# Kernel optimization log

Hardware: AMD Instinct MI355X
Metric: run time of the kernel (lower is better)

Reference implementation:

```python
import jax, jax.numpy as jnp
import numpy as np

N = 100000
E = 1600000
IN_DIM = 128
HEADS = 8
OUT_PER_HEAD = 16  # output_dim // heads = 128 // 8
NEG_SLOPE = 0.2    # PyG GATConv default negative_slope


def setup_inputs() -> dict:
    key = jax.random.key(0)
    k_x, k_ei, k_w, k_as, k_ad, k_b = jax.random.split(key, 6)
    x = jax.random.normal(k_x, (N, IN_DIM), dtype=jnp.float32)
    edge_index = jax.random.randint(k_ei, (2, E), 0, N, dtype=jnp.int64)
    # GATConv params (Glorot-ish scale)
    scale = 1.0 / np.sqrt(IN_DIM)
    W = jax.random.normal(k_w, (IN_DIM, HEADS, OUT_PER_HEAD), dtype=jnp.float32) * scale
    a_src = jax.random.normal(k_as, (HEADS, OUT_PER_HEAD), dtype=jnp.float32) * scale
    a_dst = jax.random.normal(k_ad, (HEADS, OUT_PER_HEAD), dtype=jnp.float32) * scale
    bias = jnp.zeros((HEADS * OUT_PER_HEAD,), dtype=jnp.float32)
    return {"x": x, "edge_index": edge_index, "W": W, "a_src": a_src,
            "a_dst": a_dst, "bias": bias}


def reference(x, edge_index, W, a_src, a_dst, bias):
    # Linear projection per head: [N, H, F]
    xp = jnp.einsum('ni,ihf->nhf', x, W)
    # Per-node attention halves: [N, H]
    al_src = jnp.einsum('nhf,hf->nh', xp, a_src)
    al_dst = jnp.einsum('nhf,hf->nh', xp, a_dst)
    src, dst = edge_index[0], edge_index[1]
    # Edge logits with LeakyReLU: [E, H]
    e = al_src[src] + al_dst[dst]
    e = jnp.where(e >= 0, e, NEG_SLOPE * e)
    # Segment softmax over incoming edges of each dst node
    m = jnp.full((N, HEADS), -jnp.inf, dtype=e.dtype).at[dst].max(e)
    ex = jnp.exp(e - m[dst])
    denom = jnp.zeros((N, HEADS), dtype=e.dtype).at[dst].add(ex)
    alpha = ex / jnp.where(denom[dst] == 0, 1.0, denom[dst])  # [E, H]
    # Weighted scatter-aggregate of source messages: [N, H, F]
    out = jnp.zeros((N, HEADS, OUT_PER_HEAD), dtype=xp.dtype)
    out = out.at[dst].add(xp[src] * alpha[:, :, None])
    # Concat heads, bias, ELU (GATLayer applies F.elu)
    out = out.reshape(N, HEADS * OUT_PER_HEAD) + bias
    return jnp.where(out > 0, out, jnp.expm1(out))
```

## Files before the change

kernel.cpp:

```cpp
#include <hip/hip_runtime.h>
#include <hip/hip_fp16.h>
#include <cstdint>

constexpr int IN_DIM = 128;
constexpr int OUT_DIM = 128;
constexpr int HEADS = 8;
constexpr float NEG_SLOPE = 0.2f;

constexpr int BUCKET_CAP = 2560;
constexpr int BIN_TILE   = 2048;

typedef _Float16 f16x8 __attribute__((ext_vector_type(8)));
typedef float    f32x4 __attribute__((ext_vector_type(4)));

__global__ void wa_kernel(const float* __restrict__ W, const float* __restrict__ a_src,
                          const float* __restrict__ a_dst, __half* __restrict__ wa) {
  int k = threadIdx.x;
  if (k < 128) {
#pragma unroll
    for (int h = 0; h < 8; ++h) {
      float s = 0.f, d = 0.f;
#pragma unroll
      for (int f = 0; f < 16; ++f) {
        float w = W[k * 128 + h * 16 + f];
        s += w * a_src[h * 16 + f];
        d += w * a_dst[h * 16 + f];
      }
      wa[k * 16 + h]     = __float2half(s);
      wa[k * 16 + 8 + h] = __float2half(d);
    }
  }
}

__global__ __launch_bounds__(256) void proj_kernel(
    const float* __restrict__ x, const float* __restrict__ W,
    const __half* __restrict__ wa, __half* __restrict__ xp,
    float* __restrict__ als, float* __restrict__ ald, int N)
{
  __shared__ __half xs[64 * 128];
  __shared__ __half Wt[144 * 128];
  const int t  = threadIdx.x;
  const int r0 = blockIdx.x * 64;

#pragma unroll
  for (int it = 0; it < 4; ++it) {
    int m   = t + it * 256;
    int row = m >> 4;
    int g   = m & 15;
    int grow = r0 + row;
    float4 v0 = make_float4(0.f,0.f,0.f,0.f), v1 = v0;
    if (grow < N) {
      const float* src = &x[(size_t)grow * IN_DIM + g * 8];
      v0 = *(const float4*)src;
      v1 = *(const float4*)(src + 4);
    }
    union { __half2 h2[4]; uint4 u; } u;
    u.h2[0] = __floats2half2_rn(v0.x, v0.y);
    u.h2[1] = __floats2half2_rn(v0.z, v0.w);
    u.h2[2] = __floats2half2_rn(v1.x, v1.y);
    u.h2[3] = __floats2half2_rn(v1.z, v1.w);
    *(uint4*)&xs[row * 128 + ((g ^ (row & 15)) << 3)] = u.u;
  }
#pragma unroll
  for (int it = 0; it < 16; ++it) {
    int m  = t + it * 256;
    int c  = m & 127;
    int kq = m >> 7;
    int k  = kq * 4;
    float w0 = W[(size_t)(k + 0) * OUT_DIM + c];
    float w1 = W[(size_t)(k + 1) * OUT_DIM + c];
    float w2 = W[(size_t)(k + 2) * OUT_DIM + c];
    float w3 = W[(size_t)(k + 3) * OUT_DIM + c];
    union { __half2 h2[2]; uint2 u; } u;
    u.h2[0] = __floats2half2_rn(w0, w1);
    u.h2[1] = __floats2half2_rn(w2, w3);
    int g = k >> 3;
    *(uint2*)&Wt[c * 128 + (((g ^ (c & 15)) << 3) + (k & 7))] = u.u;
  }
#pragma unroll
  for (int it = 0; it < 2; ++it) {
    int m  = t + it * 256;
    int c  = m & 15;
    int kq = m >> 4;
    int k  = kq * 4;
    union { __half h[4]; uint2 u; } u;
    u.h[0] = wa[(k + 0) * 16 + c];
    u.h[1] = wa[(k + 1) * 16 + c];
    u.h[2] = wa[(k + 2) * 16 + c];
    u.h[3] = wa[(k + 3) * 16 + c];
    int cc = 128 + c;
    int g = k >> 3;
    *(uint2*)&Wt[cc * 128 + (((g ^ (cc & 15)) << 3) + (k & 7))] = u.u;
  }
  __syncthreads();

  const int wv = t >> 6;
  const int l  = t & 63;
  const int fr = l & 15;
  const int fq = l >> 4;

  f32x4 acc[9];
#pragma unroll
  for (int ct = 0; ct < 9; ++ct) acc[ct] = (f32x4){0.f,0.f,0.f,0.f};

#pragma unroll
  for (int ks = 0; ks < 4; ++ks) {
    int g = 4 * ks + fq;
    f16x8 a = *(const f16x8*)&xs[(16 * wv + fr) * 128 + ((g ^ fr) << 3)];
#pragma unroll
    for (int ct = 0; ct < 9; ++ct) {
      f16x8 b = *(const f16x8*)&Wt[(16 * ct + fr) * 128 + ((g ^ fr) << 3)];
      acc[ct] = __builtin_amdgcn_mfma_f32_16x16x32_f16(a, b, acc[ct], 0, 0, 0);
    }
  }
  __syncthreads();

#pragma unroll
  for (int r = 0; r < 4; ++r) {
    int grow = r0 + 16 * wv + 4 * fq + r;
    if (grow < N) {
      float v = acc[8][r];
      if (fr < 8) als[grow * HEADS + fr] = v;
      else        ald[grow * HEADS + (fr - 8)] = v;
    }
  }

#pragma unroll
  for (int ct = 0; ct < 8; ++ct)
#pragma unroll
    for (int r = 0; r < 4; ++r)
      xs[(16 * wv + 4 * fq + r) * 128 + 16 * ct + fr] = __float2half(acc[ct][r]);
  __syncthreads();

#pragma unroll
  for (int it = 0; it < 4; ++it) {
    int m   = t + it * 256;
    int row = m >> 4;
    int u4  = m & 15;
    int grow = r0 + row;
    if (grow < N) {
      uint4 v = *(const uint4*)&xs[row * 128 + u4 * 8];
      *(uint4*)&xp[(size_t)grow * OUT_DIM + u4 * 8] = v;
    }
  }
}

__global__ void detect_kernel(const void* __restrict__ ei, int E, int N,
                              int* __restrict__ flag) {
  const long long* e64 = (const long long*)ei;
  int lane = threadIdx.x;
  int step = E > 64 ? E / 64 : 1;
  size_t idx = ((size_t)lane * step) % (size_t)E;
  long long v = e64[idx];
  int bad = (v < 0 || v >= (long long)N) ? 1 : 0;
  unsigned long long m = __ballot(bad);
  if (lane == 0) *flag = (m == 0ull) ? 1 : 0;
}

__device__ __forceinline__ int load_idx(const void* ei, size_t i, int is64) {
  return is64 ? (int)((const long long*)ei)[i] : ((const int*)ei)[i];
}

__global__ __launch_bounds__(256) void bin_kernel(
    const void* __restrict__ ei, const int* __restrict__ flag,
    int* __restrict__ bucket_cnt, unsigned int* __restrict__ buckets,
    int E)
{
  __shared__ int cnt[1024];
  const int is64 = *flag;
  const int t = threadIdx.x;
#pragma unroll
  for (int b = t; b < 1024; b += 256) cnt[b] = 0;
  __syncthreads();

  unsigned int rec[8];
  short bk[8];
  const int base_e = blockIdx.x * BIN_TILE;
#pragma unroll
  for (int j = 0; j < 8; ++j) {
    int idx = base_e + j * 256 + t;
    bk[j] = -1;
    if (idx < E) {
      int s = load_idx(ei, (size_t)idx, is64);
      int d = load_idx(ei, (size_t)E + idx, is64);
      rec[j] = ((unsigned)(d & 127) << 24) | (unsigned)s;
      bk[j] = (short)(d >> 7);
      atomicAdd(&cnt[d >> 7], 1);
    }
  }
  __syncthreads();

#pragma unroll
  for (int b = t; b < 1024; b += 256) {
    int c = cnt[b];
    cnt[b] = (c > 0) ? atomicAdd(&bucket_cnt[b], c) : 0;
  }
  __syncthreads();

#pragma unroll
  for (int j = 0; j < 8; ++j) {
    if (bk[j] >= 0) {
      int pos = atomicAdd(&cnt[bk[j]], 1);
      if (pos < BUCKET_CAP)
        buckets[(size_t)bk[j] * BUCKET_CAP + pos] = rec[j];
    }
  }
}

__global__ __launch_bounds__(1024) void bucket_scan(const int* __restrict__ bucket_cnt,
                                                    int* __restrict__ bucket_base) {
  __shared__ int lds[1024];
  int t = threadIdx.x;
  int v = bucket_cnt[t];
  lds[t] = v;
  __syncthreads();
  for (int d = 1; d < 1024; d <<= 1) {
    int u = (t >= d) ? lds[t - d] : 0;
    __syncthreads();
    lds[t] += u;
    __syncthreads();
  }
  bucket_base[t] = lds[t] - v;
  if (t == 1023) bucket_base[1024] = lds[1023];
}

__global__ __launch_bounds__(256) void sort_bucket(
    const unsigned int* __restrict__ buckets, const int* __restrict__ bucket_base,
    int* __restrict__ csr, int* __restrict__ row_off, int N, int E)
{
  __shared__ unsigned int recs[BUCKET_CAP];
  __shared__ int cnt[128];
  __shared__ int sc[128];
  const int b = blockIdx.x;
  const int t = threadIdx.x;
  const int base = bucket_base[b];
  int m = bucket_base[b + 1] - base;
  if (m > BUCKET_CAP) m = BUCKET_CAP;

  if (t < 128) cnt[t] = 0;
  __syncthreads();
  for (int i = t; i < m; i += 256) {
    unsigned int r = buckets[(size_t)b * BUCKET_CAP + i];
    recs[i] = r;
    atomicAdd(&cnt[r >> 24], 1);
  }
  __syncthreads();

  if (t < 128) sc[t] = cnt[t];
  __syncthreads();
  for (int d = 1; d < 128; d <<= 1) {
    int u = (t < 128 && t >= d) ? sc[t - d] : 0;
    __syncthreads();
    if (t < 128) sc[t] += u;
    __syncthreads();
  }
  int excl = (t < 128) ? sc[t] - cnt[t] : 0;

  int n = (b << 7) + t;
  if (t < 128 && n < N) row_off[n] = base + excl;
  if (b == 0 && t == 0) row_off[N] = E;

  if (t < 128) cnt[t] = base + excl;
  __syncthreads();
  for (int i = t; i < m; i += 256) {
    unsigned int r = recs[i];
    int pos = atomicAdd(&cnt[r >> 24], 1);
    csr[pos] = (int)(r & 0x00FFFFFFu);
  }
}

__global__ __launch_bounds__(256) void aggregate_kernel(
    const __half* __restrict__ xp, const float* __restrict__ als,
    const float* __restrict__ ald, const int* __restrict__ row_off,
    const int* __restrict__ csr, const float* __restrict__ bias,
    float* __restrict__ out, int N)
{
  int node = blockIdx.x * 4 + (threadIdx.x >> 6);
  if (node >= N) return;
  const int lane = threadIdx.x & 63;
  const int j = lane & 7;
  const int h = lane >> 3;
  const float ad = ald[node * HEADS + h];
  int beg = row_off[node], end = row_off[node + 1];
  beg = __builtin_amdgcn_readfirstlane(beg);
  end = __builtin_amdgcn_readfirstlane(end);

  float acc0 = 0.f, acc1 = 0.f, den_p = 0.f;
  int i = beg;
  const int nfull = (end - beg) >> 3;
  if (nfull > 0) {
    int s_cur = csr[i + j];
    float e0 = als[s_cur * HEADS + h] + ad;
    float w_cur = __expf(fmaxf(e0, NEG_SLOPE * e0));
    for (int c = 1; c < nfull; ++c) {
      int s_nxt = csr[i + 8 + j];
      float as_n = als[s_nxt * HEADS + h];
      den_p += w_cur;
#pragma unroll
      for (int q = 0; q < 8; ++q) {
        int   sq = __shfl(s_cur, q);
        float wq = __shfl(w_cur, (lane & 56) | q);
        float2 f = __half22float2(*(const __half2*)&xp[(size_t)sq * OUT_DIM + 2 * lane]);
        acc0 = fmaf(wq, f.x, acc0);
        acc1 = fmaf(wq, f.y, acc1);
      }
      float en = as_n + ad;
      w_cur = __expf(fmaxf(en, NEG_SLOPE * en));
      s_cur = s_nxt;
      i += 8;
    }
    den_p += w_cur;
#pragma unroll
    for (int q = 0; q < 8; ++q) {
      int   sq = __shfl(s_cur, q);
      float wq = __shfl(w_cur, (lane & 56) | q);
      float2 f = __half22float2(*(const __half2*)&xp[(size_t)sq * OUT_DIM + 2 * lane]);
      acc0 = fmaf(wq, f.x, acc0);
      acc1 = fmaf(wq, f.y, acc1);
    }
    i += 8;
  }
  if (i < end) {
    int rem = end - i;
    int idx = i + j;
    int s = csr[idx < end ? idx : i];
    float e = als[s * HEADS + h] + ad;
    float w = (j < rem) ? __expf(fmaxf(e, NEG_SLOPE * e)) : 0.f;
    den_p += w;
    for (int q = 0; q < rem; ++q) {
      int   sq = __shfl(s, q);
      float wq = __shfl(w, (lane & 56) | q);
      float2 f = __half22float2(*(const __half2*)&xp[(size_t)sq * OUT_DIM + 2 * lane]);
      acc0 = fmaf(wq, f.x, acc0);
      acc1 = fmaf(wq, f.y, acc1);
    }
  }
  den_p += __shfl_xor(den_p, 1);
  den_p += __shfl_xor(den_p, 2);
  den_p += __shfl_xor(den_p, 4);

  float inv = den_p > 0.f ? 1.f / den_p : 0.f;
  float2 b = *(const float2*)&bias[2 * lane];
  float v0 = fmaf(acc0, inv, b.x);
  float v1 = fmaf(acc1, inv, b.y);
  float2 o;
  o.x = v0 > 0.f ? v0 : expm1f(v0);
  o.y = v1 > 0.f ? v1 : expm1f(v1);
  *(float2*)&out[(size_t)node * OUT_DIM + 2 * lane] = o;
}

extern "C" void kernel_launch(void* const* d_in, const int* in_sizes, int n_in,
                              void* d_out, int out_size, void* d_ws, size_t ws_size,
                              hipStream_t stream) {
  const float* x      = (const float*)d_in[0];
  const void*  ei     = d_in[1];
  const float* W      = (const float*)d_in[2];
  const float* a_src  = (const float*)d_in[3];
  const float* a_dst  = (const float*)d_in[4];
  const float* bias   = (const float*)d_in[5];
  float* out = (float*)d_out;
  const int N = in_sizes[0] / IN_DIM;
  const int E = in_sizes[1] / 2;
  const int NB  = (N + 127) >> 7;
  const int nbt = (E + BIN_TILE - 1) / BIN_TILE;

  char* ws = (char*)d_ws;
  size_t off = 0;
  __half* xp          = (__half*)(ws + off); off += (size_t)N * OUT_DIM * 2;
  off = (off + 15) & ~(size_t)15;
  float* als          = (float*)(ws + off);  off += (size_t)N * HEADS * 4;
  float* ald          = (float*)(ws + off);  off += (size_t)N * HEADS * 4;
  __half* wa          = (__half*)(ws + off); off += 128 * 16 * 2;
  int*   bucket_cnt   = (int*)(ws + off);    off += 1024 * 4;
  int*   bucket_base  = (int*)(ws + off);    off += 1028 * 4;
  unsigned int* buckets = (unsigned int*)(ws + off); off += (size_t)1024 * BUCKET_CAP * 4;
  int*   csr          = (int*)(ws + off);    off += (size_t)E * 4;
  int*   row_off      = (int*)(ws + off);    off += ((size_t)N + 4) * 4;
  int*   flag         = (int*)(ws + off);    off += 16;

  hipMemsetAsync(bucket_cnt, 0, 1024 * 4, stream);
  detect_kernel<<<1, 64, 0, stream>>>(ei, E, N, flag);
  wa_kernel<<<1, 128, 0, stream>>>(W, a_src, a_dst, wa);

  proj_kernel<<<(N + 63) / 64, 256, 0, stream>>>(x, W, wa, xp, als, ald, N);

  bin_kernel<<<nbt, 256, 0, stream>>>(ei, flag, bucket_cnt, buckets, E);
  bucket_scan<<<1, 1024, 0, stream>>>(bucket_cnt, bucket_base);
  sort_bucket<<<NB, 256, 0, stream>>>(buckets, bucket_base, csr, row_off, N, E);
  aggregate_kernel<<<(N + 3) / 4, 256, 0, stream>>>(xp, als, ald, row_off, csr,
                                                    bias, out, N);
}
```

Baseline: 257.7 us.

## Store xp and attention logits head-major and split aggregation per head

Changes xp, als and ald from node-major to head-major layout, so each head's 16-feature slice is a contiguous 32-byte row. The aggregate kernel now launches 8x more blocks, one head per block, and each wave processes 4 edges in parallel across 16-lane groups followed by a cross-group reduction. The aim is to keep each head's gather table smaller and more cache-resident and to remove the shuffle-heavy inner loop. In exchange, csr and row_off are re-read once per head, and each gather fetches only 32 bytes, which may waste memory transactions. Nontemporal stores and loads are also added.

```diff
diff --git a/kernel.cpp b/kernel.cpp
--- a/kernel.cpp
+++ b/kernel.cpp
@@ -12,6 +12,7 @@
 
 typedef _Float16 f16x8 __attribute__((ext_vector_type(8)));
 typedef float    f32x4 __attribute__((ext_vector_type(4)));
+typedef unsigned int u32x4 __attribute__((ext_vector_type(4)));
 
 __global__ void wa_kernel(const float* __restrict__ W, const float* __restrict__ a_src,
                           const float* __restrict__ a_dst, __half* __restrict__ wa) {
@@ -120,8 +121,8 @@
     int grow = r0 + 16 * wv + 4 * fq + r;
     if (grow < N) {
       float v = acc[8][r];
-      if (fr < 8) als[grow * HEADS + fr] = v;
-      else        ald[grow * HEADS + (fr - 8)] = v;
+      if (fr < 8) als[(size_t)fr * N + grow] = v;
+      else        ald[(size_t)(fr - 8) * N + grow] = v;
     }
   }
 
@@ -134,13 +135,16 @@
 
 #pragma unroll
   for (int it = 0; it < 4; ++it) {
-    int m   = t + it * 256;
-    int row = m >> 4;
-    int u4  = m & 15;
+    int tt   = t + it * 256;
+    int head = tt >> 7;
+    int rem  = tt & 127;
+    int row  = rem >> 1;
+    int g16  = rem & 1;
     int grow = r0 + row;
     if (grow < N) {
-      uint4 v = *(const uint4*)&xs[row * 128 + u4 * 8];
-      *(uint4*)&xp[(size_t)grow * OUT_DIM + u4 * 8] = v;
+      u32x4 v = *(const u32x4*)&xs[row * 128 + head * 16 + g16 * 8];
+      __builtin_nontemporal_store(v,
+        (u32x4*)&xp[((size_t)head * N + grow) * 16 + g16 * 8]);
     }
   }
 }
@@ -270,83 +274,67 @@
 }
 
 __global__ __launch_bounds__(256) void aggregate_kernel(
-    const __half* __restrict__ xp, const float* __restrict__ als,
-    const float* __restrict__ ald, const int* __restrict__ row_off,
+    const __half* __restrict__ xp,
+    const float* __restrict__ als,
+    const float* __restrict__ ald,
+    const int* __restrict__ row_off,
     const int* __restrict__ csr, const float* __restrict__ bias,
     float* __restrict__ out, int N)
 {
-  int node = blockIdx.x * 4 + (threadIdx.x >> 6);
+  const int h = blockIdx.x & 7;
+  const int g = blockIdx.x >> 3;
+  const int node = g * 4 + (threadIdx.x >> 6);
   if (node >= N) return;
   const int lane = threadIdx.x & 63;
-  const int j = lane & 7;
-  const int h = lane >> 3;
-  const float ad = ald[node * HEADS + h];
+  const int j = lane >> 4;
+  const int f = lane & 15;
+  const float* als_h = als + (size_t)h * N;
+  const __half* xp_h = xp + (size_t)h * N * 16;
+  const float ad = ald[(size_t)h * N + node];
   int beg = row_off[node], end = row_off[node + 1];
   beg = __builtin_amdgcn_readfirstlane(beg);
   end = __builtin_amdgcn_readfirstlane(end);
 
-  float acc0 = 0.f, acc1 = 0.f, den_p = 0.f;
+  float acc = 0.f, den = 0.f;
   int i = beg;
-  const int nfull = (end - beg) >> 3;
-  if (nfull > 0) {
-    int s_cur = csr[i + j];
-    float e0 = als[s_cur * HEADS + h] + ad;
-    float w_cur = __expf(fmaxf(e0, NEG_SLOPE * e0));
-    for (int c = 1; c < nfull; ++c) {
-      int s_nxt = csr[i + 8 + j];
-      float as_n = als[s_nxt * HEADS + h];
-      den_p += w_cur;
-#pragma unroll
-      for (int q = 0; q < 8; ++q) {
-        int   sq = __shfl(s_cur, q);
-        float wq = __shfl(w_cur, (lane & 56) | q);
-        float2 f = __half22float2(*(const __half2*)&xp[(size_t)sq * OUT_DIM + 2 * lane]);
-        acc0 = fmaf(wq, f.x, acc0);
-        acc1 = fmaf(wq, f.y, acc1);
-      }
-      float en = as_n + ad;
-      w_cur = __expf(fmaxf(en, NEG_SLOPE * en));
-      s_cur = s_nxt;
-      i += 8;
-    }
-    den_p += w_cur;
-#pragma unroll
-    for (int q = 0; q < 8; ++q) {
-      int   sq = __shfl(s_cur, q);
-      float wq = __shfl(w_cur, (lane & 56) | q);
-      float2 f = __half22float2(*(const __half2*)&xp[(size_t)sq * OUT_DIM + 2 * lane]);
-      acc0 = fmaf(wq, f.x, acc0);
-      acc1 = fmaf(wq, f.y, acc1);
-    }
-    i += 8;
+  for (; i + 8 <= end; i += 8) {
+    int sa = __builtin_nontemporal_load(&csr[i + j]);
+    int sb = __builtin_nontemporal_load(&csr[i + 4 + j]);
+    float ea = als_h[sa] + ad;
+    float eb = als_h[sb] + ad;
+    float wa = __expf(fmaxf(ea, NEG_SLOPE * ea));
+    float wb = __expf(fmaxf(eb, NEG_SLOPE * eb));
+    float xa = __half2float(xp_h[(size_t)sa * 16 + f]);
+    float xb = __half2float(xp_h[(size_t)sb * 16 + f]);
+    den += wa + wb;
+    acc = fmaf(wa, xa, acc);
+    acc = fmaf(wb, xb, acc);
   }
   if (i < end) {
     int rem = end - i;
-    int idx = i + j;
-    int s = csr[idx < end ? idx : i];
-    float e = als[s * HEADS + h] + ad;
-    float w = (j < rem) ? __expf(fmaxf(e, NEG_SLOPE * e)) : 0.f;
-    den_p += w;
-    for (int q = 0; q < rem; ++q) {
-      int   sq = __shfl(s, q);
-      float wq = __shfl(w, (lane & 56) | q);
-      float2 f = __half22float2(*(const __half2*)&xp[(size_t)sq * OUT_DIM + 2 * lane]);
-      acc0 = fmaf(wq, f.x, acc0);
-      acc1 = fmaf(wq, f.y, acc1);
-    }
-  }
-  den_p += __shfl_xor(den_p, 1);
-  den_p += __shfl_xor(den_p, 2);
-  den_p += __shfl_xor(den_p, 4);
-
-  float inv = den_p > 0.f ? 1.f / den_p : 0.f;
-  float2 b = *(const float2*)&bias[2 * lane];
-  float v0 = fmaf(acc0, inv, b.x);
-  float v1 = fmaf(acc1, inv, b.y);
-  float2 o;
-  o.x = v0 > 0.f ? v0 : expm1f(v0);
-  o.y = v1 > 0.f ? v1 : expm1f(v1);
-  *(float2*)&out[(size_t)node * OUT_DIM + 2 * lane] = o;
+    int va = (j < rem), vb = (j + 4 < rem);
+    int sa = __builtin_nontemporal_load(&csr[va ? i + j : i]);
+    int sb = __builtin_nontemporal_load(&csr[vb ? i + 4 + j : i]);
+    float ea = als_h[sa] + ad;
+    float eb = als_h[sb] + ad;
+    float wa = va ? __expf(fmaxf(ea, NEG_SLOPE * ea)) : 0.f;
+    float wb = vb ? __expf(fmaxf(eb, NEG_SLOPE * eb)) : 0.f;
+    float xa = __half2float(xp_h[(size_t)sa * 16 + f]);
+    float xb = __half2float(xp_h[(size_t)sb * 16 + f]);
+    den += wa + wb;
+    acc = fmaf(wa, xa, acc);
+    acc = fmaf(wb, xb, acc);
+  }
+  acc += __shfl_xor(acc, 16); acc += __shfl_xor(acc, 32);
+  den += __shfl_xor(den, 16); den += __shfl_xor(den, 32);
+
+  if (j == 0) {
+    float inv = den > 0.f ? 1.f / den : 0.f;
+    float b = bias[h * 16 + f];
+    float v = fmaf(acc, inv, b);
+    float o = v > 0.f ? v : expm1f(v);
+    __builtin_nontemporal_store(o, &out[(size_t)node * OUT_DIM + h * 16 + f]);
+  }
 }
 
 extern "C" void kernel_launch(void* const* d_in, const int* in_sizes, int n_in,
@@ -387,6 +375,6 @@
   bin_kernel<<<nbt, 256, 0, stream>>>(ei, flag, bucket_cnt, buckets, E);
   bucket_scan<<<1, 1024, 0, stream>>>(bucket_cnt, bucket_base);
   sort_bucket<<<NB, 256, 0, stream>>>(buckets, bucket_base, csr, row_off, N, E);
-  aggregate_kernel<<<(N + 3) / 4, 256, 0, stream>>>(xp, als, ald, row_off, csr,
-                                                    bias, out, N);
-}
+  aggregate_kernel<<<((N + 3) / 4) * 8, 256, 0, stream>>>(xp, als, ald, row_off,
+                                                          csr, bias, out, N);
+}
```

Result: slower. 526.1 us (+104.2%).
